# Performance work log

Measured on AMD Instinct MI355X. Metric: run time of the kernel, lower is better.

The kernel has to match this reference:

```python
import jax, jax.numpy as jnp
import numpy as np

D_MODEL = 512
D_FF = 2048
N_HEADS = 8
D_HEAD = D_MODEL // N_HEADS
EPS = 1e-6
NEG = -1e9


def setup_inputs() -> dict:
    key = jax.random.key(0)
    ks = jax.random.split(key, 16)
    B, S = 4, 2048
    w = lambda k, sh: jax.random.normal(k, sh, dtype=jnp.float32) * 0.02
    return {
        "x": jax.random.normal(ks[0], (B, S, D_MODEL), dtype=jnp.float32),
        "mask": jax.random.randint(ks[1], (B, S, S), 0, 2).astype(bool),
        "gamma1": jnp.ones((D_MODEL,), jnp.float32),
        "beta1": jnp.zeros((D_MODEL,), jnp.float32),
        "Wq": w(ks[2], (D_MODEL, D_MODEL)), "bq": jnp.zeros((D_MODEL,), jnp.float32),
        "Wk": w(ks[3], (D_MODEL, D_MODEL)), "bk": jnp.zeros((D_MODEL,), jnp.float32),
        "Wv": w(ks[4], (D_MODEL, D_MODEL)), "bv": jnp.zeros((D_MODEL,), jnp.float32),
        "Wo": w(ks[5], (D_MODEL, D_MODEL)), "bo": jnp.zeros((D_MODEL,), jnp.float32),
        "gamma2": jnp.ones((D_MODEL,), jnp.float32),
        "beta2": jnp.zeros((D_MODEL,), jnp.float32),
        "W1": w(ks[6], (D_MODEL, D_FF)), "b1": jnp.zeros((D_FF,), jnp.float32),
        "W2": w(ks[7], (D_FF, D_MODEL)), "b2": jnp.zeros((D_MODEL,), jnp.float32),
    }


def _layer_norm(x, gamma, beta):
    # Faithful to the torch module: uses std with Bessel correction (ddof=1)
    # and divides by (sigma + eps), NOT sqrt(var + eps).
    mu = jnp.mean(x, axis=-1, keepdims=True)
    sigma = jnp.std(x, axis=-1, keepdims=True, ddof=1)
    return gamma * (x - mu) / (sigma + EPS) + beta


def _self_attention(x, mask, Wq, bq, Wk, bk, Wv, bv, Wo, bo):
    B, S, _ = x.shape
    # [B,S,D] -> [B,H,S,Dh]
    split = lambda t: t.reshape(B, S, N_HEADS, D_HEAD).transpose(0, 2, 1, 3)
    Q = split(x @ Wq + bq)
    K = split(x @ Wk + bk)
    V = split(x @ Wv + bv)
    scores = jnp.einsum("bhqd,bhkd->bhqk", Q, K) / jnp.sqrt(jnp.float32(D_HEAD))
    # masked_fill(mask == 0, -1e9): keep where mask True
    scores = jnp.where(mask[:, None, :, :], scores, NEG)
    attn = jax.nn.softmax(scores, axis=-1)
    ctx = jnp.einsum("bhqk,bhkd->bhqd", attn, V)  # [B,H,S,Dh]
    ctx = ctx.transpose(0, 2, 1, 3).reshape(B, S, D_MODEL)
    return ctx @ Wo + bo


def reference(x, mask, gamma1, beta1, Wq, bq, Wk, bk, Wv, bv, Wo, bo,
              gamma2, beta2, W1, b1, W2, b2):
    # pre-layer-norm encoder block (dropout = identity in eval)
    h = _layer_norm(x, gamma1, beta1)
    x = x + _self_attention(h, mask, Wq, bq, Wk, bk, Wv, bv, Wo, bo)
    h2 = _layer_norm(x, gamma2, beta2)
    ff = jax.nn.relu(h2 @ W1 + b1) @ W2 + b2
    return x + ff
```

## Files before the change

### kernel.cpp

```cpp
#include <hip/hip_runtime.h>
#include <hip/hip_bf16.h>
#include <math.h>

#define D_MODEL 512
#define D_FF    2048
#define N_HEADS 8
#define D_HEAD  64
#define BATCH   4
#define SEQ     2048
#define NROWS   (BATCH * SEQ)
#define LN_EPS  1e-6f

typedef __attribute__((ext_vector_type(8))) short s8b;
typedef __attribute__((ext_vector_type(4))) float f4;
typedef unsigned int u32;
typedef unsigned short u16;

__device__ inline u16 f2bf(float f) {
    u32 u = __float_as_uint(f);
    return (u16)((u + 0x7fffu + ((u >> 16) & 1u)) >> 16);
}
__device__ inline float bf2f(u16 h) {
    return __uint_as_float(((u32)h) << 16);
}

__device__ inline f4 mfma16(s8b a, s8b b, f4 c) {
    return __builtin_amdgcn_mfma_f32_16x16x32_bf16(a, b, c, 0, 0, 0);
}

__device__ inline void gload16(const u16* g, u16* lds) {
    __builtin_amdgcn_global_load_lds(
        (const __attribute__((address_space(1))) unsigned int*)g,
        (__attribute__((address_space(3))) unsigned int*)lds, 16, 0, 0);
}

__global__ __launch_bounds__(256) void ln_kernel(
    const float* __restrict__ in, const float* __restrict__ gamma,
    const float* __restrict__ beta, u16* __restrict__ out)
{
    const int row = blockIdx.x;
    const int t = threadIdx.x;
    const float* x = in + (size_t)row * D_MODEL;

    float2 v = *(const float2*)(x + t * 2);
    float s = v.x + v.y, ss = v.x * v.x + v.y * v.y;
    #pragma unroll
    for (int m = 1; m < 64; m <<= 1) { s += __shfl_xor(s, m); ss += __shfl_xor(ss, m); }
    __shared__ float red[8];
    const int wid = t >> 6;
    if ((t & 63) == 0) { red[wid] = s; red[wid + 4] = ss; }
    __syncthreads();
    const float st  = red[0] + red[1] + red[2] + red[3];
    const float sst = red[4] + red[5] + red[6] + red[7];
    const float mu  = st / (float)D_MODEL;
    float var = fmaxf((sst - (float)D_MODEL * mu * mu) / (float)(D_MODEL - 1), 0.f);
    const float inv = 1.f / (sqrtf(var) + LN_EPS);
    const float2 g = *(const float2*)(gamma + t * 2);
    const float2 b = *(const float2*)(beta + t * 2);
    u32 o = (u32)f2bf(g.x * (v.x - mu) * inv + b.x)
          | ((u32)f2bf(g.y * (v.y - mu) * inv + b.y) << 16);
    *(u32*)(out + (size_t)row * D_MODEL + t * 2) = o;
}

__global__ __launch_bounds__(256) void packmask_kernel(
    const int* __restrict__ mask, u32* __restrict__ bits)
{
    const int w = blockIdx.x * 256 + threadIdx.x;
    const int* p = mask + (size_t)w * 32;
    u32 b = 0;
    #pragma unroll
    for (int i = 0; i < 8; ++i) {
        int4 v = *(const int4*)(p + i * 4);
        b |= (v.x ? 1u : 0u) << (i * 4 + 0);
        b |= (v.y ? 1u : 0u) << (i * 4 + 1);
        b |= (v.z ? 1u : 0u) << (i * 4 + 2);
        b |= (v.w ? 1u : 0u) << (i * 4 + 3);
    }
    bits[w] = b;
}

__global__ __launch_bounds__(256) void splitw_kernel(
    const float* __restrict__ W, u16* __restrict__ Wh, u16* __restrict__ Wl,
    int K, int N)
{
    __shared__ float tile[32][33];
    const int k0 = blockIdx.x * 32, n0 = blockIdx.y * 32;
    const int t = threadIdx.x;
    const int r = t >> 3, c4 = (t & 7) * 4;
    *(float4*)&tile[r][c4] = *(const float4*)(W + (size_t)(k0 + r) * N + n0 + c4);
    __syncthreads();
    u16 hh[4], ll[4];
    #pragma unroll
    for (int j = 0; j < 4; ++j) {
        float v = tile[c4 + j][r];
        hh[j] = f2bf(v);
        ll[j] = f2bf(v - bf2f(hh[j]));
    }
    size_t o = (size_t)(n0 + r) * K + k0 + c4;
    *(u32*)(Wh + o)     = (u32)hh[0] | ((u32)hh[1] << 16);
    *(u32*)(Wh + o + 2) = (u32)hh[2] | ((u32)hh[3] << 16);
    *(u32*)(Wl + o)     = (u32)ll[0] | ((u32)ll[1] << 16);
    *(u32*)(Wl + o + 2) = (u32)ll[2] | ((u32)ll[3] << 16);
}

template<int MODE>
__global__ __launch_bounds__(256, 2) void gemm_kernel(
    const u16* __restrict__ A, const u16* __restrict__ Bh,
    const u16* __restrict__ Bl, const float* __restrict__ bias,
    const float* __restrict__ resid, void* __restrict__ Cv,
    int M, int N, int K)
{
    __shared__ u16 As[128 * 64];
    __shared__ u16 Bhs[128 * 64];
    __shared__ u16 Bls[128 * 64];

    const int tid = threadIdx.x;
    const int lane = tid & 63;
    const int wv = tid >> 6;
    const int wr = wv >> 1, wc = wv & 1;
    const int g = lane >> 4, l15 = lane & 15;
    const int bm = blockIdx.x * 128, bn = blockIdx.y * 128;

    const int srow = lane >> 3;
    const int scol = ((lane & 7) ^ srow) * 8;

    f4 acc[4][4];
    #pragma unroll
    for (int i = 0; i < 4; ++i)
        #pragma unroll
        for (int j = 0; j < 4; ++j) acc[i][j] = (f4){0.f, 0.f, 0.f, 0.f};

    for (int kt = 0; kt < K; kt += 64) {
        #pragma unroll
        for (int i = 0; i < 4; ++i) {
            const int r0 = wv * 32 + i * 8;
            gload16(A  + (size_t)(bm + r0 + srow) * K + kt + scol, As  + r0 * 64);
            gload16(Bh + (size_t)(bn + r0 + srow) * K + kt + scol, Bhs + r0 * 64);
            gload16(Bl + (size_t)(bn + r0 + srow) * K + kt + scol, Bls + r0 * 64);
        }
        __syncthreads();
        #pragma unroll
        for (int kh = 0; kh < 2; ++kh) {
            s8b af[4], bhf[4], blf[4];
            #pragma unroll
            for (int rb = 0; rb < 4; ++rb) {
                const int row = wr * 64 + rb * 16 + l15;
                af[rb] = *(const s8b*)&As[row * 64 + ((kh * 4 + g) ^ (row & 7)) * 8];
            }
            #pragma unroll
            for (int cf = 0; cf < 4; ++cf) {
                const int row = wc * 64 + cf * 16 + l15;
                const int ko = ((kh * 4 + g) ^ (row & 7)) * 8;
                bhf[cf] = *(const s8b*)&Bhs[row * 64 + ko];
                blf[cf] = *(const s8b*)&Bls[row * 64 + ko];
            }
            #pragma unroll
            for (int rb = 0; rb < 4; ++rb)
                #pragma unroll
                for (int cf = 0; cf < 4; ++cf) {
                    acc[rb][cf] = mfma16(af[rb], bhf[cf], acc[rb][cf]);
                    acc[rb][cf] = mfma16(af[rb], blf[cf], acc[rb][cf]);
                }
        }
        __syncthreads();
    }

    #pragma unroll
    for (int rb = 0; rb < 4; ++rb)
        #pragma unroll
        for (int cf = 0; cf < 4; ++cf) {
            const int col = bn + wc * 64 + cf * 16 + l15;
            const float bv = bias[col];
            #pragma unroll
            for (int r = 0; r < 4; ++r) {
                const int row = bm + wr * 64 + rb * 16 + 4 * g + r;
                float v = acc[rb][cf][r] + bv;
                if (MODE == 0) {
                    const int b_ = row >> 11, s_ = row & (SEQ - 1);
                    const int h_ = col >> 6, d_ = col & 63;
                    ((u16*)Cv)[(((size_t)(b_ * N_HEADS + h_) * SEQ + s_) << 6) + d_] = f2bf(v);
                } else if (MODE == 1) {
                    const int b_ = row >> 11, s_ = row & (SEQ - 1);
                    const int h_ = col >> 6, d_ = col & 63;
                    ((u16*)Cv)[(((size_t)(b_ * N_HEADS + h_) * 64 + d_) << 11) + s_] = f2bf(v);
                } else if (MODE == 2) {
                    ((u16*)Cv)[(size_t)row * N + col] = f2bf(fmaxf(v, 0.f));
                } else {
                    ((float*)Cv)[(size_t)row * N + col] = v + resid[(size_t)row * N + col];
                }
            }
        }
}

__global__ __launch_bounds__(256, 2) void flash_kernel(
    const u16* __restrict__ Q,
    const u16* __restrict__ Kg,
    const u16* __restrict__ Vt,
    const u32* __restrict__ mbits,
    u16* __restrict__ ctx)
{
    __shared__ u16 Qs[128 * 72];
    __shared__ u16 Ps[128 * 72];

    const int tid = threadIdx.x;
    const int lane = tid & 63;
    const int w = tid >> 6;
    const int g = lane >> 4, l15 = lane & 15;

    const int bid = blockIdx.x;
    const int local = bid >> 3;
    const int bh = (bid & 7) * 4 + (local >> 4);
    const int qt = local & 15;
    const int q0 = qt * 128;
    const int b_ = bh >> 3, h_ = bh & 7;

    const u16* Qb = Q  + (size_t)bh * SEQ * 64;
    const u16* Kb = Kg + (size_t)bh * SEQ * 64;
    const u16* Vb = Vt + (size_t)bh * 64 * SEQ;

    #pragma unroll
    for (int i = 0; i < 4; ++i) {
        const int c = i * 256 + tid;
        const int row = c >> 3, cb = (c & 7) * 8;
        *(s8b*)&Qs[row * 72 + cb] = *(const s8b*)(Qb + (size_t)(q0 + row) * 64 + cb);
    }
    __syncthreads();

    s8b qf[2][2];
    #pragma unroll
    for (int rb = 0; rb < 2; ++rb)
        #pragma unroll
        for (int kh = 0; kh < 2; ++kh)
            qf[rb][kh] = *(const s8b*)&Qs[(w * 32 + rb * 16 + l15) * 72 + kh * 32 + g * 8];

    f4 o[2][4];
    float lsum[2][4];
    #pragma unroll
    for (int rb = 0; rb < 2; ++rb) {
        #pragma unroll
        for (int df = 0; df < 4; ++df) o[rb][df] = (f4){0.f, 0.f, 0.f, 0.f};
        #pragma unroll
        for (int r = 0; r < 4; ++r) lsum[rb][r] = 0.f;
    }

    for (int kv0 = 0; kv0 < SEQ; kv0 += 64) {
        f4 s[2][4];
        #pragma unroll
        for (int rb = 0; rb < 2; ++rb)
            #pragma unroll
            for (int cf = 0; cf < 4; ++cf) s[rb][cf] = (f4){0.f, 0.f, 0.f, 0.f};

        #pragma unroll
        for (int kh = 0; kh < 2; ++kh) {
            s8b kf[4];
            #pragma unroll
            for (int cf = 0; cf < 4; ++cf)
                kf[cf] = *(const s8b*)(Kb + (size_t)(kv0 + cf * 16 + l15) * 64 + kh * 32 + g * 8);
            #pragma unroll
            for (int rb = 0; rb < 2; ++rb)
                #pragma unroll
                for (int cf = 0; cf < 4; ++cf)
                    s[rb][cf] = mfma16(qf[rb][kh], kf[cf], s[rb][cf]);
        }

        #pragma unroll
        for (int rb = 0; rb < 2; ++rb)
            #pragma unroll
            for (int r = 0; r < 4; ++r) {
                const int qrow = q0 + w * 32 + rb * 16 + 4 * g + r;
                const uint2 mw = *(const uint2*)(mbits + ((size_t)b_ * SEQ + qrow) * 64 + (kv0 >> 5));
                #pragma unroll
                for (int cf = 0; cf < 4; ++cf) {
                    const u32 word = (cf < 2) ? mw.x : mw.y;
                    const u32 bit = (word >> ((cf & 1) * 16 + l15)) & 1u;
                    float p = bit ? __expf(s[rb][cf][r] * 0.125f) : 0.f;
                    lsum[rb][r] += p;
                    Ps[(size_t)(w * 32 + rb * 16 + 4 * g + r) * 72 + cf * 16 + l15] = f2bf(p);
                }
            }
        asm volatile("s_waitcnt lgkmcnt(0)" ::: "memory");

        #pragma unroll
        for (int kh = 0; kh < 2; ++kh) {
            s8b pf[2], vf[4];
            #pragma unroll
            for (int rb = 0; rb < 2; ++rb)
                pf[rb] = *(const s8b*)&Ps[(w * 32 + rb * 16 + l15) * 72 + kh * 32 + g * 8];
            #pragma unroll
            for (int df = 0; df < 4; ++df)
                vf[df] = *(const s8b*)(Vb + (size_t)(df * 16 + l15) * SEQ + kv0 + kh * 32 + g * 8);
            #pragma unroll
            for (int rb = 0; rb < 2; ++rb)
                #pragma unroll
                for (int df = 0; df < 4; ++df)
                    o[rb][df] = mfma16(pf[rb], vf[df], o[rb][df]);
        }
    }

    #pragma unroll
    for (int rb = 0; rb < 2; ++rb)
        #pragma unroll
        for (int r = 0; r < 4; ++r) {
            float L = lsum[rb][r];
            L += __shfl_xor(L, 1); L += __shfl_xor(L, 2);
            L += __shfl_xor(L, 4); L += __shfl_xor(L, 8);
            const float invl = 1.f / L;
            const int qrow = q0 + w * 32 + rb * 16 + 4 * g + r;
            #pragma unroll
            for (int df = 0; df < 4; ++df)
                ctx[((size_t)b_ * SEQ + qrow) * D_MODEL + h_ * 64 + df * 16 + l15] =
                    f2bf(o[rb][df][r] * invl);
        }
}

extern "C" void kernel_launch(void* const* d_in, const int* in_sizes, int n_in,
                              void* d_out, int out_size, void* d_ws, size_t ws_size,
                              hipStream_t stream)
{
    const float* x      = (const float*)d_in[0];
    const int*   mask   = (const int*)  d_in[1];
    const float* gamma1 = (const float*)d_in[2];
    const float* beta1  = (const float*)d_in[3];
    const float* Wq = (const float*)d_in[4];  const float* bq = (const float*)d_in[5];
    const float* Wk = (const float*)d_in[6];  const float* bk = (const float*)d_in[7];
    const float* Wv = (const float*)d_in[8];  const float* bv = (const float*)d_in[9];
    const float* Wo = (const float*)d_in[10]; const float* bo = (const float*)d_in[11];
    const float* gamma2 = (const float*)d_in[12];
    const float* beta2  = (const float*)d_in[13];
    const float* W1 = (const float*)d_in[14]; const float* b1 = (const float*)d_in[15];
    const float* W2 = (const float*)d_in[16]; const float* b2 = (const float*)d_in[17];
    float* out = (float*)d_out;

    char* ws = (char*)d_ws;
    const size_t MB = 1ull << 20;
    u16* h    = (u16*)(ws);
    u16* Qb   = (u16*)(ws + 8 * MB);
    u16* Kb   = (u16*)(ws + 16 * MB);
    u16* Vtb  = (u16*)(ws + 24 * MB);
    u16* ctx  = (u16*)(ws + 32 * MB);
    u16* hid  = (u16*)(ws + 8 * MB);
    float* y  = (float*)(ws + 40 * MB);
    u32* mb   = (u32*)(ws + 56 * MB);
    u16* Wqh = (u16*)(ws + 58 * MB);          u16* Wql = (u16*)(ws + 58 * MB + 512 * 1024);
    u16* Wkh = (u16*)(ws + 59 * MB);          u16* Wkl = (u16*)(ws + 59 * MB + 512 * 1024);
    u16* Wvh = (u16*)(ws + 60 * MB);          u16* Wvl = (u16*)(ws + 60 * MB + 512 * 1024);
    u16* Woh = (u16*)(ws + 61 * MB);          u16* Wol = (u16*)(ws + 61 * MB + 512 * 1024);
    u16* W1h = (u16*)(ws + 62 * MB);          u16* W1l = (u16*)(ws + 64 * MB);
    u16* W2h = (u16*)(ws + 66 * MB);          u16* W2l = (u16*)(ws + 68 * MB);

    const dim3 blk(256);
    const dim3 gP(NROWS / 128, D_MODEL / 128);
    const dim3 gF(NROWS / 128, D_FF / 128);

    packmask_kernel<<<(BATCH * SEQ * SEQ / 32) / 256, blk, 0, stream>>>(mask, mb);
    splitw_kernel<<<dim3(16, 16), blk, 0, stream>>>(Wq, Wqh, Wql, 512, 512);
    splitw_kernel<<<dim3(16, 16), blk, 0, stream>>>(Wk, Wkh, Wkl, 512, 512);
    splitw_kernel<<<dim3(16, 16), blk, 0, stream>>>(Wv, Wvh, Wvl, 512, 512);
    splitw_kernel<<<dim3(16, 16), blk, 0, stream>>>(Wo, Woh, Wol, 512, 512);
    splitw_kernel<<<dim3(16, 64), blk, 0, stream>>>(W1, W1h, W1l, 512, 2048);
    splitw_kernel<<<dim3(64, 16), blk, 0, stream>>>(W2, W2h, W2l, 2048, 512);

    ln_kernel<<<NROWS, blk, 0, stream>>>(x, gamma1, beta1, h);
    gemm_kernel<0><<<gP, blk, 0, stream>>>(h, Wqh, Wql, bq, nullptr, Qb, NROWS, D_MODEL, D_MODEL);
    gemm_kernel<0><<<gP, blk, 0, stream>>>(h, Wkh, Wkl, bk, nullptr, Kb, NROWS, D_MODEL, D_MODEL);
    gemm_kernel<1><<<gP, blk, 0, stream>>>(h, Wvh, Wvl, bv, nullptr, Vtb, NROWS, D_MODEL, D_MODEL);
    flash_kernel<<<512, blk, 0, stream>>>(Qb, Kb, Vtb, mb, ctx);
    gemm_kernel<3><<<gP, blk, 0, stream>>>(ctx, Woh, Wol, bo, x, y, NROWS, D_MODEL, D_MODEL);
    ln_kernel<<<NROWS, blk, 0, stream>>>(y, gamma2, beta2, h);
    gemm_kernel<2><<<gF, blk, 0, stream>>>(h, W1h, W1l, b1, nullptr, hid, NROWS, D_FF, D_MODEL);
    gemm_kernel<3><<<gP, blk, 0, stream>>>(hid, W2h, W2l, b2, y, out, NROWS, D_MODEL, D_FF);
}
```

Before: 480.6 us.

## Split flash attention KV range across wave pairs with LDS partial-sum combine

The flash kernel now uses 64-row query tiles and splits the KV sequence in half between two wave pairs. Partial outputs and row sums are combined through shared memory at the end, and the grid doubles to 1024 blocks to give more parallelism and occupancy. It also switches to exp2f with a folded scale, uses the hardware bf16 conversion for P, and raises the launch-bounds occupancy hints on the gemm and flash kernels. The cost is an extra combine step and synchronisation, plus possible register pressure from the higher occupancy targets.

```diff
diff --git a/kernel.cpp b/kernel.cpp
--- a/kernel.cpp
+++ b/kernel.cpp
@@ -22,6 +22,10 @@
 }
 __device__ inline float bf2f(u16 h) {
     return __uint_as_float(((u32)h) << 16);
+}
+__device__ inline u16 f2bf_hw(float f) {
+    __hip_bfloat16 hb = __float2bfloat16(f);
+    return *reinterpret_cast<u16*>(&hb);
 }
 
 __device__ inline f4 mfma16(s8b a, s8b b, f4 c) {
@@ -104,7 +108,7 @@
 }
 
 template<int MODE>
-__global__ __launch_bounds__(256, 2) void gemm_kernel(
+__global__ __launch_bounds__(256, 3) void gemm_kernel(
     const u16* __restrict__ A, const u16* __restrict__ Bh,
     const u16* __restrict__ Bl, const float* __restrict__ bias,
     const float* __restrict__ resid, void* __restrict__ Cv,
@@ -192,26 +196,29 @@
         }
 }
 
-__global__ __launch_bounds__(256, 2) void flash_kernel(
+__global__ __launch_bounds__(256, 4) void flash_kernel(
     const u16* __restrict__ Q,
     const u16* __restrict__ Kg,
     const u16* __restrict__ Vt,
     const u32* __restrict__ mbits,
     u16* __restrict__ ctx)
 {
-    __shared__ u16 Qs[128 * 72];
-    __shared__ u16 Ps[128 * 72];
+    __shared__ __align__(16) u16 smem[13824];
+    u16* Qs = smem;
+    u16* Ps = smem + 64 * 72;
 
     const int tid = threadIdx.x;
     const int lane = tid & 63;
     const int w = tid >> 6;
     const int g = lane >> 4, l15 = lane & 15;
+    const int rowgrp = (w & 1) * 32;
+    const int kvbase = (w >> 1) * (SEQ / 2);
 
     const int bid = blockIdx.x;
     const int local = bid >> 3;
-    const int bh = (bid & 7) * 4 + (local >> 4);
-    const int qt = local & 15;
-    const int q0 = qt * 128;
+    const int bh = (bid & 7) * 4 + (local >> 5);
+    const int qt = local & 31;
+    const int q0 = qt * 64;
     const int b_ = bh >> 3, h_ = bh & 7;
 
     const u16* Qb = Q  + (size_t)bh * SEQ * 64;
@@ -219,7 +226,7 @@
     const u16* Vb = Vt + (size_t)bh * 64 * SEQ;
 
     #pragma unroll
-    for (int i = 0; i < 4; ++i) {
+    for (int i = 0; i < 2; ++i) {
         const int c = i * 256 + tid;
         const int row = c >> 3, cb = (c & 7) * 8;
         *(s8b*)&Qs[row * 72 + cb] = *(const s8b*)(Qb + (size_t)(q0 + row) * 64 + cb);
@@ -231,7 +238,7 @@
     for (int rb = 0; rb < 2; ++rb)
         #pragma unroll
         for (int kh = 0; kh < 2; ++kh)
-            qf[rb][kh] = *(const s8b*)&Qs[(w * 32 + rb * 16 + l15) * 72 + kh * 32 + g * 8];
+            qf[rb][kh] = *(const s8b*)&Qs[(rowgrp + rb * 16 + l15) * 72 + kh * 32 + g * 8];
 
     f4 o[2][4];
     float lsum[2][4];
@@ -243,7 +250,10 @@
         for (int r = 0; r < 4; ++r) lsum[rb][r] = 0.f;
     }
 
-    for (int kv0 = 0; kv0 < SEQ; kv0 += 64) {
+    const int psbase = w * 32 * 72;
+
+    for (int it = 0; it < (SEQ / 2) / 64; ++it) {
+        const int kv0 = kvbase + it * 64;
         f4 s[2][4];
         #pragma unroll
         for (int rb = 0; rb < 2; ++rb)
@@ -267,15 +277,16 @@
         for (int rb = 0; rb < 2; ++rb)
             #pragma unroll
             for (int r = 0; r < 4; ++r) {
-                const int qrow = q0 + w * 32 + rb * 16 + 4 * g + r;
+                const int qrow = q0 + rowgrp + rb * 16 + 4 * g + r;
                 const uint2 mw = *(const uint2*)(mbits + ((size_t)b_ * SEQ + qrow) * 64 + (kv0 >> 5));
+                const int prow = psbase + (rb * 16 + 4 * g + r) * 72;
                 #pragma unroll
                 for (int cf = 0; cf < 4; ++cf) {
                     const u32 word = (cf < 2) ? mw.x : mw.y;
                     const u32 bit = (word >> ((cf & 1) * 16 + l15)) & 1u;
-                    float p = bit ? __expf(s[rb][cf][r] * 0.125f) : 0.f;
+                    float p = bit ? exp2f(s[rb][cf][r] * 0.18033688011117310f) : 0.f;
                     lsum[rb][r] += p;
-                    Ps[(size_t)(w * 32 + rb * 16 + 4 * g + r) * 72 + cf * 16 + l15] = f2bf(p);
+                    Ps[prow + cf * 16 + l15] = f2bf_hw(p);
                 }
             }
         asm volatile("s_waitcnt lgkmcnt(0)" ::: "memory");
@@ -285,7 +296,7 @@
             s8b pf[2], vf[4];
             #pragma unroll
             for (int rb = 0; rb < 2; ++rb)
-                pf[rb] = *(const s8b*)&Ps[(w * 32 + rb * 16 + l15) * 72 + kh * 32 + g * 8];
+                pf[rb] = *(const s8b*)&Ps[psbase + (rb * 16 + l15) * 72 + kh * 32 + g * 8];
             #pragma unroll
             for (int df = 0; df < 4; ++df)
                 vf[df] = *(const s8b*)(Vb + (size_t)(df * 16 + l15) * SEQ + kv0 + kh * 32 + g * 8);
@@ -297,20 +308,54 @@
         }
     }
 
-    #pragma unroll
-    for (int rb = 0; rb < 2; ++rb)
-        #pragma unroll
-        for (int r = 0; r < 4; ++r) {
-            float L = lsum[rb][r];
-            L += __shfl_xor(L, 1); L += __shfl_xor(L, 2);
-            L += __shfl_xor(L, 4); L += __shfl_xor(L, 8);
-            const float invl = 1.f / L;
-            const int qrow = q0 + w * 32 + rb * 16 + 4 * g + r;
+    float* combf = (float*)smem;
+    __syncthreads();
+    if (w >= 2) {
+        const int base = ((w - 2) * 64 + lane) * 41;
+        #pragma unroll
+        for (int rb = 0; rb < 2; ++rb)
             #pragma unroll
             for (int df = 0; df < 4; ++df)
-                ctx[((size_t)b_ * SEQ + qrow) * D_MODEL + h_ * 64 + df * 16 + l15] =
-                    f2bf(o[rb][df][r] * invl);
-        }
+                #pragma unroll
+                for (int r = 0; r < 4; ++r)
+                    combf[base + (rb * 4 + df) * 4 + r] = o[rb][df][r];
+        #pragma unroll
+        for (int rb = 0; rb < 2; ++rb)
+            #pragma unroll
+            for (int r = 0; r < 4; ++r)
+                combf[base + 32 + rb * 4 + r] = lsum[rb][r];
+    }
+    __syncthreads();
+    if (w < 2) {
+        const int base = (w * 64 + lane) * 41;
+        #pragma unroll
+        for (int rb = 0; rb < 2; ++rb)
+            #pragma unroll
+            for (int df = 0; df < 4; ++df)
+                #pragma unroll
+                for (int r = 0; r < 4; ++r)
+                    o[rb][df][r] += combf[base + (rb * 4 + df) * 4 + r];
+        #pragma unroll
+        for (int rb = 0; rb < 2; ++rb)
+            #pragma unroll
+            for (int r = 0; r < 4; ++r)
+                lsum[rb][r] += combf[base + 32 + rb * 4 + r];
+
+        #pragma unroll
+        for (int rb = 0; rb < 2; ++rb)
+            #pragma unroll
+            for (int r = 0; r < 4; ++r) {
+                float L = lsum[rb][r];
+                L += __shfl_xor(L, 1); L += __shfl_xor(L, 2);
+                L += __shfl_xor(L, 4); L += __shfl_xor(L, 8);
+                const float invl = 1.f / L;
+                const int qrow = q0 + rowgrp + rb * 16 + 4 * g + r;
+                #pragma unroll
+                for (int df = 0; df < 4; ++df)
+                    ctx[((size_t)b_ * SEQ + qrow) * D_MODEL + h_ * 64 + df * 16 + l15] =
+                        f2bf(o[rb][df][r] * invl);
+            }
+    }
 }
 
 extern "C" void kernel_launch(void* const* d_in, const int* in_sizes, int n_in,
@@ -364,7 +409,7 @@
     gemm_kernel<0><<<gP, blk, 0, stream>>>(h, Wqh, Wql, bq, nullptr, Qb, NROWS, D_MODEL, D_MODEL);
     gemm_kernel<0><<<gP, blk, 0, stream>>>(h, Wkh, Wkl, bk, nullptr, Kb, NROWS, D_MODEL, D_MODEL);
     gemm_kernel<1><<<gP, blk, 0, stream>>>(h, Wvh, Wvl, bv, nullptr, Vtb, NROWS, D_MODEL, D_MODEL);
-    flash_kernel<<<512, blk, 0, stream>>>(Qb, Kb, Vtb, mb, ctx);
+    flash_kernel<<<1024, blk, 0, stream>>>(Qb, Kb, Vtb, mb, ctx);
     gemm_kernel<3><<<gP, blk, 0, stream>>>(ctx, Woh, Wol, bo, x, y, NROWS, D_MODEL, D_MODEL);
     ln_kernel<<<NROWS, blk, 0, stream>>>(y, gamma2, beta2, h);
     gemm_kernel<2><<<gF, blk, 0, stream>>>(h, W1h, W1l, b1, nullptr, hid, NROWS, D_FF, D_MODEL);
```

Result: slower. 531.0 us (+10.5%).

## Software-pipeline K loads and hoist V/mask loads in flash attention loop

Applied to the files above, without the earlier changes.

Restructures the flash attention inner loop to double-buffer K fragments in registers: the next tile's K is loaded while the current tile's scores are processed. V fragments and mask words are issued at the start of each iteration, and the loop is unrolled by two via an inlined body with swapped buffers. It also switches exp to exp2f with a folded scale, uses the hardware bf16 conversion, and raises GEMM launch-bound occupancy to 3 blocks. This adds register pressure at 2 blocks/SM, which risks spills or reduced occupancy.

```diff
diff --git a/kernel.cpp b/kernel.cpp
--- a/kernel.cpp
+++ b/kernel.cpp
@@ -22,6 +22,10 @@
 }
 __device__ inline float bf2f(u16 h) {
     return __uint_as_float(((u32)h) << 16);
+}
+__device__ inline u16 f2bf_hw(float f) {
+    __hip_bfloat16 hb = __float2bfloat16(f);
+    return *reinterpret_cast<u16*>(&hb);
 }
 
 __device__ inline f4 mfma16(s8b a, s8b b, f4 c) {
@@ -104,7 +108,7 @@
 }
 
 template<int MODE>
-__global__ __launch_bounds__(256, 2) void gemm_kernel(
+__global__ __launch_bounds__(256, 3) void gemm_kernel(
     const u16* __restrict__ A, const u16* __restrict__ Bh,
     const u16* __restrict__ Bl, const float* __restrict__ bias,
     const float* __restrict__ resid, void* __restrict__ Cv,
@@ -192,6 +196,82 @@
         }
 }
 
+struct FlashCtx {
+    const u16* Kb; const u16* Vb; const u32* Mb; u16* Ps;
+    int psbase, l15, g;
+};
+
+__device__ __forceinline__ void flash_body(
+    const FlashCtx& cx, int it,
+    const s8b (&qf)[2][2], const s8b (&kfC)[2][4], s8b (&kfN)[2][4],
+    f4 (&o)[2][4], float (&lsum)[2][4])
+{
+    const int kv0 = it * 64;
+    const int kvn = (it == 31) ? 0 : kv0 + 64;
+    const int l15 = cx.l15, g = cx.g;
+
+    s8b vf[2][4];
+    #pragma unroll
+    for (int kh = 0; kh < 2; ++kh)
+        #pragma unroll
+        for (int df = 0; df < 4; ++df)
+            vf[kh][df] = *(const s8b*)(cx.Vb + (size_t)(df * 16 + l15) * SEQ + kv0 + kh * 32 + g * 8);
+
+    uint2 mw[2][4];
+    #pragma unroll
+    for (int rb = 0; rb < 2; ++rb)
+        #pragma unroll
+        for (int r = 0; r < 4; ++r)
+            mw[rb][r] = *(const uint2*)(cx.Mb + (rb * 16 + 4 * g + r) * 64 + (kv0 >> 5));
+
+    f4 s[2][4];
+    #pragma unroll
+    for (int rb = 0; rb < 2; ++rb)
+        #pragma unroll
+        for (int cf = 0; cf < 4; ++cf) s[rb][cf] = (f4){0.f, 0.f, 0.f, 0.f};
+    #pragma unroll
+    for (int kh = 0; kh < 2; ++kh)
+        #pragma unroll
+        for (int rb = 0; rb < 2; ++rb)
+            #pragma unroll
+            for (int cf = 0; cf < 4; ++cf)
+                s[rb][cf] = mfma16(qf[rb][kh], kfC[kh][cf], s[rb][cf]);
+
+    #pragma unroll
+    for (int kh = 0; kh < 2; ++kh)
+        #pragma unroll
+        for (int cf = 0; cf < 4; ++cf)
+            kfN[kh][cf] = *(const s8b*)(cx.Kb + (size_t)(kvn + cf * 16 + l15) * 64 + kh * 32 + g * 8);
+
+    #pragma unroll
+    for (int rb = 0; rb < 2; ++rb)
+        #pragma unroll
+        for (int r = 0; r < 4; ++r) {
+            const int prow = cx.psbase + (rb * 16 + 4 * g + r) * 72;
+            #pragma unroll
+            for (int cf = 0; cf < 4; ++cf) {
+                const u32 word = (cf < 2) ? mw[rb][r].x : mw[rb][r].y;
+                const u32 bit = (word >> ((cf & 1) * 16 + l15)) & 1u;
+                float p = bit ? exp2f(s[rb][cf][r] * 0.18033688011117310f) : 0.f;
+                lsum[rb][r] += p;
+                cx.Ps[prow + cf * 16 + l15] = f2bf_hw(p);
+            }
+        }
+    asm volatile("s_waitcnt lgkmcnt(0)" ::: "memory");
+
+    #pragma unroll
+    for (int kh = 0; kh < 2; ++kh) {
+        s8b pf[2];
+        pf[0] = *(const s8b*)&cx.Ps[cx.psbase + l15 * 72 + kh * 32 + g * 8];
+        pf[1] = *(const s8b*)&cx.Ps[cx.psbase + (16 + l15) * 72 + kh * 32 + g * 8];
+        #pragma unroll
+        for (int rb = 0; rb < 2; ++rb)
+            #pragma unroll
+            for (int df = 0; df < 4; ++df)
+                o[rb][df] = mfma16(pf[rb], vf[kh][df], o[rb][df]);
+    }
+}
+
 __global__ __launch_bounds__(256, 2) void flash_kernel(
     const u16* __restrict__ Q,
     const u16* __restrict__ Kg,
@@ -199,8 +279,8 @@
     const u32* __restrict__ mbits,
     u16* __restrict__ ctx)
 {
-    __shared__ u16 Qs[128 * 72];
-    __shared__ u16 Ps[128 * 72];
+    __shared__ __align__(16) u16 Qs[128 * 72];
+    __shared__ __align__(16) u16 Ps[128 * 72];
 
     const int tid = threadIdx.x;
     const int lane = tid & 63;
@@ -217,6 +297,7 @@
     const u16* Qb = Q  + (size_t)bh * SEQ * 64;
     const u16* Kb = Kg + (size_t)bh * SEQ * 64;
     const u16* Vb = Vt + (size_t)bh * 64 * SEQ;
+    const u32* Mb = mbits + ((size_t)b_ * SEQ + q0 + w * 32) * 64;
 
     #pragma unroll
     for (int i = 0; i < 4; ++i) {
@@ -243,58 +324,21 @@
         for (int r = 0; r < 4; ++r) lsum[rb][r] = 0.f;
     }
 
-    for (int kv0 = 0; kv0 < SEQ; kv0 += 64) {
-        f4 s[2][4];
-        #pragma unroll
-        for (int rb = 0; rb < 2; ++rb)
-            #pragma unroll
-            for (int cf = 0; cf < 4; ++cf) s[rb][cf] = (f4){0.f, 0.f, 0.f, 0.f};
-
-        #pragma unroll
-        for (int kh = 0; kh < 2; ++kh) {
-            s8b kf[4];
-            #pragma unroll
-            for (int cf = 0; cf < 4; ++cf)
-                kf[cf] = *(const s8b*)(Kb + (size_t)(kv0 + cf * 16 + l15) * 64 + kh * 32 + g * 8);
-            #pragma unroll
-            for (int rb = 0; rb < 2; ++rb)
-                #pragma unroll
-                for (int cf = 0; cf < 4; ++cf)
-                    s[rb][cf] = mfma16(qf[rb][kh], kf[cf], s[rb][cf]);
-        }
-
-        #pragma unroll
-        for (int rb = 0; rb < 2; ++rb)
-            #pragma unroll
-            for (int r = 0; r < 4; ++r) {
-                const int qrow = q0 + w * 32 + rb * 16 + 4 * g + r;
-                const uint2 mw = *(const uint2*)(mbits + ((size_t)b_ * SEQ + qrow) * 64 + (kv0 >> 5));
-                #pragma unroll
-                for (int cf = 0; cf < 4; ++cf) {
-                    const u32 word = (cf < 2) ? mw.x : mw.y;
-                    const u32 bit = (word >> ((cf & 1) * 16 + l15)) & 1u;
-                    float p = bit ? __expf(s[rb][cf][r] * 0.125f) : 0.f;
-                    lsum[rb][r] += p;
-                    Ps[(size_t)(w * 32 + rb * 16 + 4 * g + r) * 72 + cf * 16 + l15] = f2bf(p);
-                }
-            }
-        asm volatile("s_waitcnt lgkmcnt(0)" ::: "memory");
-
-        #pragma unroll
-        for (int kh = 0; kh < 2; ++kh) {
-            s8b pf[2], vf[4];
-            #pragma unroll
-            for (int rb = 0; rb < 2; ++rb)
-                pf[rb] = *(const s8b*)&Ps[(w * 32 + rb * 16 + l15) * 72 + kh * 32 + g * 8];
-            #pragma unroll
-            for (int df = 0; df < 4; ++df)
-                vf[df] = *(const s8b*)(Vb + (size_t)(df * 16 + l15) * SEQ + kv0 + kh * 32 + g * 8);
-            #pragma unroll
-            for (int rb = 0; rb < 2; ++rb)
-                #pragma unroll
-                for (int df = 0; df < 4; ++df)
-                    o[rb][df] = mfma16(pf[rb], vf[df], o[rb][df]);
-        }
+    FlashCtx cx;
+    cx.Kb = Kb; cx.Vb = Vb; cx.Mb = Mb; cx.Ps = Ps;
+    cx.psbase = w * 32 * 72; cx.l15 = l15; cx.g = g;
+
+    s8b kfA[2][4], kfB[2][4];
+    #pragma unroll
+    for (int kh = 0; kh < 2; ++kh)
+        #pragma unroll
+        for (int cf = 0; cf < 4; ++cf)
+            kfA[kh][cf] = *(const s8b*)(Kb + (size_t)(cf * 16 + l15) * 64 + kh * 32 + g * 8);
+
+    #pragma unroll 1
+    for (int it = 0; it < 32; it += 2) {
+        flash_body(cx, it,     qf, kfA, kfB, o, lsum);
+        flash_body(cx, it + 1, qf, kfB, kfA, o, lsum);
     }
 
     #pragma unroll
```

Measured after the change: 472.4 us. No clear change (-1.7%).
